# Performance work log

Measured on AMD Instinct MI355X. Metric: run time of the kernel, lower is better.

Reference implementation:

```python
import jax, jax.numpy as jnp
import numpy as np

B, N, D, DIM = 64, 512, 128, 128
NEG_INF = -1e9


def setup_inputs() -> dict:
    key = jax.random.key(0)
    k1, k2, k3, k4 = jax.random.split(key, 4)
    atom_query = jax.random.normal(k1, (B, N, D), dtype=jnp.float32)
    # binary atom-presence mask, broadcastable over feature dim
    mask = jax.random.randint(k2, (B, N, 1), 0, 2).astype(jnp.float32)
    s = 1.0 / np.sqrt(D)
    Wq = jax.random.normal(k3, (D, DIM), dtype=jnp.float32) * s
    Wk = jax.random.normal(k4, (D, DIM), dtype=jnp.float32) * s
    bq = jnp.zeros((DIM,), dtype=jnp.float32)
    bk = jnp.zeros((DIM,), dtype=jnp.float32)
    return {"atom_query": atom_query, "mask": mask, "Wq": Wq, "bq": bq, "Wk": Wk, "bk": bk}


def reference(atom_query, mask, Wq, bq, Wk, bk):
    # projections
    q = atom_query @ Wq + bq              # [B, N, dim]
    k = atom_query @ Wk + bk              # [B, N, dim]
    mq = mask * q                          # masked query
    mk = mask * k                          # masked key

    # energy[b,i,j] = mk[b,i] . mq[b,j], with diagonal zeroed, then summed over j.
    # sum_j energy[b,i,j] = mk[b,i] . (sum_j mq[b,j]) - mk[b,i] . mq[b,i]
    # (identical math to materializing the [B,N,N] energy and reducing)
    q_sum = mq.sum(axis=1)                                   # [B, dim]
    agg = jnp.einsum('bnd,bd->bn', mk, q_sum) - (mk * mq).sum(-1)  # [B, N]
    agg = agg[:, :, None] * mask                             # [B, N, 1]

    # euclidean normalize over atom axis (tf.linalg.normalize, axis=1)
    nrm = jnp.sqrt(jnp.sum(agg * agg, axis=1, keepdims=True))
    agg = agg / nrm

    # masked softmax over atoms
    agg = agg + (1.0 - mask) * NEG_INF
    attn = jax.nn.softmax(agg, axis=1)                       # [B, N, 1]

    # v_proj=False, kq_proj=True -> values are the key projection
    context = jnp.sum(mask * attn * k, axis=1)               # [B, dim]
    return attn, context
```

## Files before the change

### kernel.cpp

```cpp
#include <hip/hip_runtime.h>
#include <math.h>

#define NB 64
#define NN 512
#define ND 128

typedef __attribute__((ext_vector_type(8))) short short8;
typedef __attribute__((ext_vector_type(4))) float f32x4;

#define KVB_OFF   0
#define QK_OFF    (NB*NN*ND/2)
#define QSUMP_OFF (QK_OFF + NB*NN)

__device__ inline unsigned short f2bf(float x) {
    unsigned int u = __float_as_uint(x);
    return (unsigned short)((u + 0x7FFFu + ((u >> 16) & 1u)) >> 16);
}
__device__ inline float bf2f(unsigned short u) {
    return __uint_as_float(((unsigned int)u) << 16);
}

__global__ __launch_bounds__(256, 1) void proj_mfma(
    const float* __restrict__ aq, const float* __restrict__ mask,
    const float* __restrict__ Wq, const float* __restrict__ bq,
    const float* __restrict__ Wk, const float* __restrict__ bk,
    unsigned short* __restrict__ kvb, float* __restrict__ qk,
    float* __restrict__ qsum_part)
{
    __shared__ __align__(16) unsigned char sbuf[34816];
    unsigned short (*wst)[132] = (unsigned short (*)[132])sbuf;
    unsigned short (*ast)[136] = (unsigned short (*)[136])sbuf;
    __shared__ float mask_lds[128];
    __shared__ float qk_part[4][128];

    const int b    = blockIdx.x >> 2;
    const int m0   = (blockIdx.x & 3) << 7;
    const int t    = threadIdx.x;
    const int w    = t >> 6, lane = t & 63;
    const int quad = lane >> 4, l16 = lane & 15;

    short8 bfr[4][4];

    #pragma unroll
    for (int s = 0; s < 2; s++) {
        const float* Wsrc = s ? Wk : Wq;
        if (s) __syncthreads();
        {
            const float4* src = (const float4*)Wsrc;
            #pragma unroll
            for (int i = 0; i < 16; i++) {
                const int idx = t + 256*i;
                const int row = idx >> 5, c4 = idx & 31;
                const float4 v = src[idx];
                ushort4 o;
                o.x = f2bf(v.x); o.y = f2bf(v.y); o.z = f2bf(v.z); o.w = f2bf(v.w);
                *(ushort4*)&wst[row][c4*4] = o;
            }
        }
        __syncthreads();
        #pragma unroll
        for (int nt = 0; nt < 2; nt++) {
            const int col = w*32 + nt*16 + l16;
            #pragma unroll
            for (int kc = 0; kc < 4; kc++) {
                short8 v;
                #pragma unroll
                for (int j = 0; j < 8; j++)
                    v[j] = (short)wst[kc*32 + quad*8 + j][col];
                bfr[s*2 + nt][kc] = v;
            }
        }
    }
    __syncthreads();

    {
        const float4* src = (const float4*)(aq + ((size_t)b*NN + m0)*ND);
        #pragma unroll
        for (int i = 0; i < 16; i++) {
            const int idx = t + 256*i;
            const int row = idx >> 5, c4 = idx & 31;
            const float4 v = src[idx];
            ushort4 o;
            o.x = f2bf(v.x); o.y = f2bf(v.y); o.z = f2bf(v.z); o.w = f2bf(v.w);
            *(ushort4*)&ast[row][c4*4] = o;
        }
        if (t < 128) mask_lds[t] = mask[b*NN + m0 + t];
    }
    __syncthreads();

    f32x4 acc[8][4];
    #pragma unroll
    for (int m = 0; m < 8; m++)
        #pragma unroll
        for (int nt = 0; nt < 4; nt++)
            acc[m][nt] = (f32x4){0.f, 0.f, 0.f, 0.f};

    #pragma unroll
    for (int m = 0; m < 8; m++) {
        short8 afr[4];
        #pragma unroll
        for (int kc = 0; kc < 4; kc++)
            afr[kc] = *(const short8*)&ast[m*16 + l16][kc*32 + quad*8];
        #pragma unroll
        for (int nt = 0; nt < 4; nt++)
            #pragma unroll
            for (int kc = 0; kc < 4; kc++)
                acc[m][nt] = __builtin_amdgcn_mfma_f32_16x16x32_bf16(
                    afr[kc], bfr[nt][kc], acc[m][nt], 0, 0, 0);
    }

    float bv[4];
    #pragma unroll
    for (int nt = 0; nt < 2; nt++) bv[nt] = bq[w*32 + nt*16 + l16];
    #pragma unroll
    for (int nt = 2; nt < 4; nt++) bv[nt] = bk[w*32 + (nt-2)*16 + l16];
    #pragma unroll
    for (int m = 0; m < 8; m++)
        #pragma unroll
        for (int nt = 0; nt < 4; nt++)
            #pragma unroll
            for (int r = 0; r < 4; r++)
                acc[m][nt][r] += bv[nt];

    #pragma unroll
    for (int m = 0; m < 8; m++)
        #pragma unroll
        for (int r = 0; r < 4; r++) {
            const size_t row = (size_t)b*NN + m0 + m*16 + quad*4 + r;
            kvb[row*ND + w*32 + l16]      = f2bf(acc[m][2][r]);
            kvb[row*ND + w*32 + 16 + l16] = f2bf(acc[m][3][r]);
        }

    #pragma unroll
    for (int m = 0; m < 8; m++) {
        float p[4];
        #pragma unroll
        for (int r = 0; r < 4; r++)
            p[r] = acc[m][0][r]*acc[m][2][r] + acc[m][1][r]*acc[m][3][r];
        #pragma unroll
        for (int off = 1; off <= 8; off <<= 1)
            #pragma unroll
            for (int r = 0; r < 4; r++)
                p[r] += __shfl_xor(p[r], off);
        if (l16 == 0)
            #pragma unroll
            for (int r = 0; r < 4; r++)
                qk_part[w][m*16 + quad*4 + r] = p[r];
    }

    {
        float s0 = 0.f, s1 = 0.f;
        #pragma unroll
        for (int m = 0; m < 8; m++)
            #pragma unroll
            for (int r = 0; r < 4; r++) {
                const float mk = mask_lds[m*16 + quad*4 + r];
                s0 += mk * acc[m][0][r];
                s1 += mk * acc[m][1][r];
            }
        s0 += __shfl_xor(s0, 16); s0 += __shfl_xor(s0, 32);
        s1 += __shfl_xor(s1, 16); s1 += __shfl_xor(s1, 32);
        if (quad == 0) {
            const int slot = blockIdx.x * ND;
            qsum_part[slot + w*32 + l16]      = s0;
            qsum_part[slot + w*32 + 16 + l16] = s1;
        }
    }

    __syncthreads();
    if (t < 128)
        qk[(size_t)b*NN + m0 + t] =
            qk_part[0][t] + qk_part[1][t] + qk_part[2][t] + qk_part[3][t];
}

__global__ __launch_bounds__(512) void fused_attn(
    const float* __restrict__ mask, const unsigned short* __restrict__ kvb,
    const float* __restrict__ qk, const float* __restrict__ qsum_part,
    float* __restrict__ out_attn, float* __restrict__ out_ctx)
{
    __shared__ float qs[128];
    __shared__ float mask_s[512];
    __shared__ float agg_s[512];
    __shared__ float red[16];
    __shared__ float bc2[2];
    __shared__ float zred[8];
    __shared__ float zbc;
    __shared__ float ctx_part[32][33];

    const int b  = blockIdx.x >> 2;
    const int cg = blockIdx.x & 3;
    const int t = threadIdx.x, w = t >> 6, lane = t & 63;
    const size_t rowbase = (size_t)b * NN;

    if (t < 128)
        qs[t] = qsum_part[(b*4 + 0)*ND + t] + qsum_part[(b*4 + 1)*ND + t]
              + qsum_part[(b*4 + 2)*ND + t] + qsum_part[(b*4 + 3)*ND + t];
    mask_s[t] = mask[rowbase + t];
    __syncthreads();

    const int h = lane & 15, quad = lane >> 4;
    float qsf[8];
    #pragma unroll
    for (int j = 0; j < 8; j++) qsf[j] = qs[h*8 + j];

    for (int i0 = 0; i0 < 64; i0 += 4) {
        const int n = w*64 + i0 + quad;
        const short8 kr = *(const short8*)(kvb + (rowbase + n)*ND + h*8);
        float p = 0.f;
        #pragma unroll
        for (int j = 0; j < 8; j++)
            p += bf2f((unsigned short)kr[j]) * qsf[j];
        #pragma unroll
        for (int off = 1; off <= 8; off <<= 1) p += __shfl_xor(p, off);
        if (h == 0)
            agg_s[n] = mask_s[n] * (p - qk[rowbase + n]);
    }
    __syncthreads();

    const float v  = agg_s[t];
    const bool um  = mask_s[t] != 0.f;
    float sq = v * v;
    float mx = um ? v : -3.0e38f;
    #pragma unroll
    for (int off = 1; off <= 32; off <<= 1) {
        sq += __shfl_xor(sq, off);
        mx = fmaxf(mx, __shfl_xor(mx, off));
    }
    if (lane == 0) { red[w] = sq; red[8 + w] = mx; }
    __syncthreads();
    if (t == 0) {
        float s = 0.f, m = -3.0e38f;
        #pragma unroll
        for (int i = 0; i < 8; i++) { s += red[i]; m = fmaxf(m, red[8 + i]); }
        bc2[0] = sqrtf(s);
        bc2[1] = m;
    }
    __syncthreads();
    const float nrm = bc2[0];
    const float M   = bc2[1];

    const float e = um ? expf((v - M) / nrm) : 0.f;
    float z = e;
    #pragma unroll
    for (int off = 1; off <= 32; off <<= 1) z += __shfl_xor(z, off);
    if (lane == 0) zred[w] = z;
    agg_s[t] = e;
    __syncthreads();
    if (t == 0) {
        float s = 0.f;
        #pragma unroll
        for (int i = 0; i < 8; i++) s += zred[i];
        zbc = s;
    }
    __syncthreads();
    const float Z = zbc;
    if (cg == 0) out_attn[rowbase + t] = e / Z;

    const int c2  = (t & 15) * 2;
    const int col = cg*32 + c2;
    const int rg  = t >> 4;
    float a0 = 0.f, a1 = 0.f;
    for (int n = rg; n < NN; n += 32) {
        const ushort2 kk = *(const ushort2*)(kvb + (rowbase + n)*ND + col);
        const float ev = agg_s[n];
        a0 += ev * bf2f(kk.x);
        a1 += ev * bf2f(kk.y);
    }
    ctx_part[rg][c2]     = a0;
    ctx_part[rg][c2 + 1] = a1;
    __syncthreads();
    if (t < 32) {
        float s = 0.f;
        #pragma unroll
        for (int i = 0; i < 32; i++) s += ctx_part[i][t];
        out_ctx[(size_t)b*ND + cg*32 + t] = s / Z;
    }
}

extern "C" void kernel_launch(void* const* d_in, const int* in_sizes, int n_in,
                              void* d_out, int out_size, void* d_ws, size_t ws_size,
                              hipStream_t stream)
{
    const float* aq   = (const float*)d_in[0];
    const float* mask = (const float*)d_in[1];
    const float* Wq   = (const float*)d_in[2];
    const float* bq   = (const float*)d_in[3];
    const float* Wk   = (const float*)d_in[4];
    const float* bk   = (const float*)d_in[5];

    float* ws = (float*)d_ws;
    unsigned short* kvb       = (unsigned short*)(ws + KVB_OFF);
    float*          qk        = ws + QK_OFF;
    float*          qsum_part = ws + QSUMP_OFF;

    float* out_attn = (float*)d_out;
    float* out_ctx  = (float*)d_out + NB*NN;

    proj_mfma<<<dim3(256), dim3(256), 0, stream>>>(aq, mask, Wq, bq, Wk, bk,
                                                   kvb, qk, qsum_part);
    fused_attn<<<dim3(256), dim3(512), 0, stream>>>(mask, kvb, qk, qsum_part,
                                                    out_attn, out_ctx);
}
```

Measured before the change: 97.67 us.

## Double projection block to 512 threads, load weights and activations together, widen context loads

The projection kernel now runs 8 waves per block, each owning 16 output columns of both Q and K, so per-wave accumulator registers are halved and more waves can hide latency. Both weight matrices and the activation tile are staged into separate LDS arrays in one combined load phase, which removes the serialized load, sync and reload sequence. The attention kernel's context reduction reads 4 bf16 values per thread with 64 row groups instead of 2 values with 32. The cost is more LDS per block and twice as many partial sums to combine.

Result: faster. 94.04 us (-3.7%).

```diff
diff --git a/kernel.cpp b/kernel.cpp
--- a/kernel.cpp
+++ b/kernel.cpp
@@ -20,18 +20,18 @@
     return __uint_as_float(((unsigned int)u) << 16);
 }
 
-__global__ __launch_bounds__(256, 1) void proj_mfma(
+__global__ __launch_bounds__(512, 1) void proj_mfma(
     const float* __restrict__ aq, const float* __restrict__ mask,
     const float* __restrict__ Wq, const float* __restrict__ bq,
     const float* __restrict__ Wk, const float* __restrict__ bk,
     unsigned short* __restrict__ kvb, float* __restrict__ qk,
     float* __restrict__ qsum_part)
 {
-    __shared__ __align__(16) unsigned char sbuf[34816];
-    unsigned short (*wst)[132] = (unsigned short (*)[132])sbuf;
-    unsigned short (*ast)[136] = (unsigned short (*)[136])sbuf;
+    __shared__ __align__(16) unsigned short wq_st[128][132];
+    __shared__ __align__(16) unsigned short wk_st[128][132];
+    __shared__ __align__(16) unsigned short ast[128][136];
     __shared__ float mask_lds[128];
-    __shared__ float qk_part[4][128];
+    __shared__ float qk_part[8][128];
 
     const int b    = blockIdx.x >> 2;
     const int m0   = (blockIdx.x & 3) << 7;
@@ -39,61 +39,51 @@
     const int w    = t >> 6, lane = t & 63;
     const int quad = lane >> 4, l16 = lane & 15;
 
-    short8 bfr[4][4];
-
-    #pragma unroll
-    for (int s = 0; s < 2; s++) {
-        const float* Wsrc = s ? Wk : Wq;
-        if (s) __syncthreads();
-        {
-            const float4* src = (const float4*)Wsrc;
-            #pragma unroll
-            for (int i = 0; i < 16; i++) {
-                const int idx = t + 256*i;
-                const int row = idx >> 5, c4 = idx & 31;
-                const float4 v = src[idx];
-                ushort4 o;
-                o.x = f2bf(v.x); o.y = f2bf(v.y); o.z = f2bf(v.z); o.w = f2bf(v.w);
-                *(ushort4*)&wst[row][c4*4] = o;
+    {
+        const float4* asrc = (const float4*)(aq + ((size_t)b*NN + m0)*ND);
+        const float4* qsrc = (const float4*)Wq;
+        const float4* ksrc = (const float4*)Wk;
+        #pragma unroll
+        for (int i = 0; i < 8; i++) {
+            const int idx = t + 512*i;
+            const int row = idx >> 5, c4 = idx & 31;
+            const float4 va = asrc[idx];
+            const float4 vq = qsrc[idx];
+            const float4 vk = ksrc[idx];
+            ushort4 oa, oq, ok;
+            oa.x = f2bf(va.x); oa.y = f2bf(va.y); oa.z = f2bf(va.z); oa.w = f2bf(va.w);
+            oq.x = f2bf(vq.x); oq.y = f2bf(vq.y); oq.z = f2bf(vq.z); oq.w = f2bf(vq.w);
+            ok.x = f2bf(vk.x); ok.y = f2bf(vk.y); ok.z = f2bf(vk.z); ok.w = f2bf(vk.w);
+            *(ushort4*)&ast[row][c4*4]   = oa;
+            *(ushort4*)&wq_st[row][c4*4] = oq;
+            *(ushort4*)&wk_st[row][c4*4] = ok;
+        }
+        if (t < 128) mask_lds[t] = mask[b*NN + m0 + t];
+    }
+    __syncthreads();
+
+    short8 bfr[2][4];
+    {
+        const int col = w*16 + l16;
+        #pragma unroll
+        for (int kc = 0; kc < 4; kc++) {
+            short8 vq, vk;
+            #pragma unroll
+            for (int j = 0; j < 8; j++) {
+                vq[j] = (short)wq_st[kc*32 + quad*8 + j][col];
+                vk[j] = (short)wk_st[kc*32 + quad*8 + j][col];
             }
-        }
-        __syncthreads();
-        #pragma unroll
-        for (int nt = 0; nt < 2; nt++) {
-            const int col = w*32 + nt*16 + l16;
-            #pragma unroll
-            for (int kc = 0; kc < 4; kc++) {
-                short8 v;
-                #pragma unroll
-                for (int j = 0; j < 8; j++)
-                    v[j] = (short)wst[kc*32 + quad*8 + j][col];
-                bfr[s*2 + nt][kc] = v;
-            }
-        }
-    }
-    __syncthreads();
-
-    {
-        const float4* src = (const float4*)(aq + ((size_t)b*NN + m0)*ND);
-        #pragma unroll
-        for (int i = 0; i < 16; i++) {
-            const int idx = t + 256*i;
-            const int row = idx >> 5, c4 = idx & 31;
-            const float4 v = src[idx];
-            ushort4 o;
-            o.x = f2bf(v.x); o.y = f2bf(v.y); o.z = f2bf(v.z); o.w = f2bf(v.w);
-            *(ushort4*)&ast[row][c4*4] = o;
-        }
-        if (t < 128) mask_lds[t] = mask[b*NN + m0 + t];
-    }
-    __syncthreads();
-
-    f32x4 acc[8][4];
-    #pragma unroll
-    for (int m = 0; m < 8; m++)
-        #pragma unroll
-        for (int nt = 0; nt < 4; nt++)
-            acc[m][nt] = (f32x4){0.f, 0.f, 0.f, 0.f};
+            bfr[0][kc] = vq;
+            bfr[1][kc] = vk;
+        }
+    }
+
+    f32x4 acc[8][2];
+    #pragma unroll
+    for (int m = 0; m < 8; m++) {
+        acc[m][0] = (f32x4){0.f, 0.f, 0.f, 0.f};
+        acc[m][1] = (f32x4){0.f, 0.f, 0.f, 0.f};
+    }
 
     #pragma unroll
     for (int m = 0; m < 8; m++) {
@@ -102,33 +92,29 @@
         for (int kc = 0; kc < 4; kc++)
             afr[kc] = *(const short8*)&ast[m*16 + l16][kc*32 + quad*8];
         #pragma unroll
-        for (int nt = 0; nt < 4; nt++)
+        for (int nt = 0; nt < 2; nt++)
             #pragma unroll
             for (int kc = 0; kc < 4; kc++)
                 acc[m][nt] = __builtin_amdgcn_mfma_f32_16x16x32_bf16(
                     afr[kc], bfr[nt][kc], acc[m][nt], 0, 0, 0);
     }
 
-    float bv[4];
-    #pragma unroll
-    for (int nt = 0; nt < 2; nt++) bv[nt] = bq[w*32 + nt*16 + l16];
-    #pragma unroll
-    for (int nt = 2; nt < 4; nt++) bv[nt] = bk[w*32 + (nt-2)*16 + l16];
+    const float bvq = bq[w*16 + l16];
+    const float bvk = bk[w*16 + l16];
     #pragma unroll
     for (int m = 0; m < 8; m++)
         #pragma unroll
-        for (int nt = 0; nt < 4; nt++)
-            #pragma unroll
-            for (int r = 0; r < 4; r++)
-                acc[m][nt][r] += bv[nt];
+        for (int r = 0; r < 4; r++) {
+            acc[m][0][r] += bvq;
+            acc[m][1][r] += bvk;
+        }
 
     #pragma unroll
     for (int m = 0; m < 8; m++)
         #pragma unroll
         for (int r = 0; r < 4; r++) {
             const size_t row = (size_t)b*NN + m0 + m*16 + quad*4 + r;
-            kvb[row*ND + w*32 + l16]      = f2bf(acc[m][2][r]);
-            kvb[row*ND + w*32 + 16 + l16] = f2bf(acc[m][3][r]);
+            kvb[row*ND + w*16 + l16] = f2bf(acc[m][1][r]);
         }
 
     #pragma unroll
@@ -136,7 +122,7 @@
         float p[4];
         #pragma unroll
         for (int r = 0; r < 4; r++)
-            p[r] = acc[m][0][r]*acc[m][2][r] + acc[m][1][r]*acc[m][3][r];
+            p[r] = acc[m][0][r] * acc[m][1][r];
         #pragma unroll
         for (int off = 1; off <= 8; off <<= 1)
             #pragma unroll
@@ -149,28 +135,23 @@
     }
 
     {
-        float s0 = 0.f, s1 = 0.f;
+        float s0 = 0.f;
         #pragma unroll
         for (int m = 0; m < 8; m++)
             #pragma unroll
-            for (int r = 0; r < 4; r++) {
-                const float mk = mask_lds[m*16 + quad*4 + r];
-                s0 += mk * acc[m][0][r];
-                s1 += mk * acc[m][1][r];
-            }
-        s0 += __shfl_xor(s0, 16); s0 += __shfl_xor(s0, 32);
-        s1 += __shfl_xor(s1, 16); s1 += __shfl_xor(s1, 32);
-        if (quad == 0) {
-            const int slot = blockIdx.x * ND;
-            qsum_part[slot + w*32 + l16]      = s0;
-            qsum_part[slot + w*32 + 16 + l16] = s1;
-        }
+            for (int r = 0; r < 4; r++)
+                s0 += mask_lds[m*16 + quad*4 + r] * acc[m][0][r];
+        s0 += __shfl_xor(s0, 16);
+        s0 += __shfl_xor(s0, 32);
+        if (quad == 0)
+            qsum_part[blockIdx.x * ND + w*16 + l16] = s0;
     }
 
     __syncthreads();
     if (t < 128)
         qk[(size_t)b*NN + m0 + t] =
-            qk_part[0][t] + qk_part[1][t] + qk_part[2][t] + qk_part[3][t];
+            qk_part[0][t] + qk_part[1][t] + qk_part[2][t] + qk_part[3][t] +
+            qk_part[4][t] + qk_part[5][t] + qk_part[6][t] + qk_part[7][t];
 }
 
 __global__ __launch_bounds__(512) void fused_attn(
@@ -185,7 +166,7 @@
     __shared__ float bc2[2];
     __shared__ float zred[8];
     __shared__ float zbc;
-    __shared__ float ctx_part[32][33];
+    __shared__ float ctx_part[64][36];
 
     const int b  = blockIdx.x >> 2;
     const int cg = blockIdx.x & 3;
@@ -256,23 +237,27 @@
     const float Z = zbc;
     if (cg == 0) out_attn[rowbase + t] = e / Z;
 
-    const int c2  = (t & 15) * 2;
-    const int col = cg*32 + c2;
-    const int rg  = t >> 4;
-    float a0 = 0.f, a1 = 0.f;
-    for (int n = rg; n < NN; n += 32) {
-        const ushort2 kk = *(const ushort2*)(kvb + (rowbase + n)*ND + col);
+    const int c4  = (t & 7) * 4;
+    const int col = cg*32 + c4;
+    const int rg  = t >> 3;
+    float a0 = 0.f, a1 = 0.f, a2 = 0.f, a3 = 0.f;
+    for (int n = rg; n < NN; n += 64) {
+        const ushort4 kk = *(const ushort4*)(kvb + (rowbase + n)*ND + col);
         const float ev = agg_s[n];
         a0 += ev * bf2f(kk.x);
         a1 += ev * bf2f(kk.y);
-    }
-    ctx_part[rg][c2]     = a0;
-    ctx_part[rg][c2 + 1] = a1;
+        a2 += ev * bf2f(kk.z);
+        a3 += ev * bf2f(kk.w);
+    }
+    ctx_part[rg][c4]     = a0;
+    ctx_part[rg][c4 + 1] = a1;
+    ctx_part[rg][c4 + 2] = a2;
+    ctx_part[rg][c4 + 3] = a3;
     __syncthreads();
     if (t < 32) {
         float s = 0.f;
         #pragma unroll
-        for (int i = 0; i < 32; i++) s += ctx_part[i][t];
+        for (int i = 0; i < 64; i++) s += ctx_part[i][t];
         out_ctx[(size_t)b*ND + cg*32 + t] = s / Z;
     }
 }
@@ -296,7 +281,7 @@
     float* out_attn = (float*)d_out;
     float* out_ctx  = (float*)d_out + NB*NN;
 
-    proj_mfma<<<dim3(256), dim3(256), 0, stream>>>(aq, mask, Wq, bq, Wk, bk,
+    proj_mfma<<<dim3(256), dim3(512), 0, stream>>>(aq, mask, Wq, bq, Wk, bk,
                                                    kvb, qk, qsum_part);
     fused_attn<<<dim3(256), dim3(512), 0, stream>>>(mask, kvb, qk, qsum_part,
                                                     out_attn, out_ctx);
```
